# Kernel tuning notes

Hardware: AMD Instinct MI355X
Metric: run time of the kernel (lower is better)

## Reference

```python
import jax, jax.numpy as jnp
import numpy as np

B, N, E, H = 8, 1500, 3000, 256
HOPS = 3


def setup_inputs() -> dict:
    key = jax.random.key(0)
    ks = jax.random.split(key, 9)
    node_state = jax.random.normal(ks[0], (B, N, H), jnp.float32)
    edge_vec = jax.random.normal(ks[1], (B, E, H), jnp.float32)
    # sparse-ish 0/1 incidence matrices (avg ~3 nonzeros per row)
    node2edge = (jax.random.uniform(ks[2], (B, E, N)) < 0.002).astype(jnp.float32)
    edge2node = (jax.random.uniform(ks[3], (B, N, E)) < 0.002).astype(jnp.float32)
    s = 1.0 / np.sqrt(H).astype(np.float32)
    W_max = jax.random.uniform(ks[4], (H, H), jnp.float32, -s, s)        # linear_max, no bias
    W_fz = jax.random.uniform(ks[5], (4 * H, H), jnp.float32, -s, s)     # gated fusion
    b_fz = jnp.zeros((H,), jnp.float32)
    W_z = jax.random.uniform(ks[6], (2 * H, H), jnp.float32, -s, s)      # GRU gates, no bias
    W_r = jax.random.uniform(ks[7], (2 * H, H), jnp.float32, -s, s)
    W_t = jax.random.uniform(ks[8], (2 * H, H), jnp.float32, -s, s)
    return dict(node_state=node_state, edge_vec=edge_vec, node2edge=node2edge,
                edge2node=edge2node, W_max=W_max, W_fz=W_fz, b_fz=b_fz,
                W_z=W_z, W_r=W_r, W_t=W_t)


def _msg_pass(node_state, edge_vec, n2e, e2n):
    # n2e: (B,E,N), e2n: (B,N,E)
    edge_emb = jnp.einsum('ben,bnh->beh', n2e, node_state) + edge_vec   # (B,E,H)
    norm = jnp.sum(e2n, axis=2, keepdims=True) + 1.0                     # self-loop degree norm
    return (jnp.einsum('bne,beh->bnh', e2n, edge_emb) + node_state) / norm


def _gated_fusion(h, x, W_fz, b_fz):
    z = jax.nn.sigmoid(jnp.concatenate([h, x, h * x, h - x], -1) @ W_fz + b_fz)
    return (1.0 - z) * h + z * x


def _gru_step(h, x, W_z, W_r, W_t):
    hx = jnp.concatenate([h, x], -1)
    z = jax.nn.sigmoid(hx @ W_z)
    r = jax.nn.sigmoid(hx @ W_r)
    t = jnp.tanh(jnp.concatenate([r * h, x], -1) @ W_t)
    return (1.0 - z) * h + z * t


def reference(node_state, edge_vec, node2edge, edge2node, W_max, W_fz, b_fz, W_z, W_r, W_t):
    n2e_T = jnp.swapaxes(node2edge, 1, 2)   # (B,N,E)
    e2n_T = jnp.swapaxes(edge2node, 1, 2)   # (B,E,N)
    for _ in range(HOPS):
        bw = _msg_pass(node_state, edge_vec, node2edge, edge2node)
        fw = _msg_pass(node_state, edge_vec, e2n_T, n2e_T)
        agg = _gated_fusion(fw, bw, W_fz, b_fz)
        node_state = _gru_step(node_state, agg, W_z, W_r, W_t)
    # graph max pool: linear then max over nodes
    graph_embedding = jnp.max(node_state @ W_max, axis=1)[None]  # (1,B,H)
    return jnp.swapaxes(node_state, 0, 1), graph_embedding       # (N,B,H), (1,B,H)
```

## Files before the change

kernel.cpp:

```cpp
#include <hip/hip_runtime.h>
#include <hip/hip_bf16.h>
#include <stdint.h>

#define Bb 8
#define Nn 1500
#define Ee 3000
#define Hh 256
#define NHOPS 3
#define CAP 32
#define Mrows (Bb*Nn)
#define BE (Bb*Ee)
#define BN (Bb*Nn)

typedef __bf16 bf16x8 __attribute__((ext_vector_type(8)));
typedef float f32x4 __attribute__((ext_vector_type(4)));

__device__ __forceinline__ float sigmoidf_(float x){ return 1.f/(1.f+__expf(-x)); }

__device__ __forceinline__ unsigned short f2b(float f){
  union { float f; unsigned int u; } x; x.f = f;
  unsigned int r = (x.u + 0x7fffu + ((x.u >> 16) & 1u)) >> 16;
  return (unsigned short)r;
}
__device__ __forceinline__ float b2f(unsigned short u){
  union { unsigned int u; float f; } x; x.u = ((unsigned int)u) << 16;
  return x.f;
}
__device__ __forceinline__ ushort4 pack4(float4 v){
  return make_ushort4(f2b(v.x), f2b(v.y), f2b(v.z), f2b(v.w));
}
__device__ __forceinline__ float4 unpack4(ushort4 u){
  return make_float4(b2f(u.x), b2f(u.y), b2f(u.z), b2f(u.w));
}

#define GLL16(g, l) __builtin_amdgcn_global_load_lds( \
    (const __attribute__((address_space(1))) unsigned int*)(g), \
    (__attribute__((address_space(3))) unsigned int*)(l), 16, 0, 0)

__device__ __forceinline__ void elemscan(const float4* __restrict__ m4, int total4,
                                         int rowlen4, int R, int C,
                                         int* __restrict__ rowIdx, int* __restrict__ rowCnt,
                                         int* __restrict__ colIdx, int* __restrict__ colCnt,
                                         int t) {
  if (t >= total4) return;
  float4 v = m4[t];
  if (v.x == 0.f && v.y == 0.f && v.z == 0.f && v.w == 0.f) return;
  int g = t / rowlen4;
  int q = t - g * rowlen4;
  int b = g / R;
  int r = g - b * R;
  int cbase = q * 4;
  #pragma unroll
  for (int j = 0; j < 4; ++j) {
    float vv = (j == 0) ? v.x : (j == 1) ? v.y : (j == 2) ? v.z : v.w;
    if (vv != 0.f) {
      int c = cbase + j;
      int rs = atomicAdd(&rowCnt[g], 1);
      if (rs < CAP) rowIdx[(size_t)g * CAP + rs] = c;
      int cs = atomicAdd(&colCnt[b * C + c], 1);
      if (cs < CAP) colIdx[(size_t)(b * C + c) * CAP + cs] = r;
    }
  }
}

__global__ void preprocess_kernel(const float* __restrict__ n2e, const float* __restrict__ e2n,
                                  int* __restrict__ Aidx, int* __restrict__ cntA,
                                  int* __restrict__ Didx, int* __restrict__ cntD,
                                  int* __restrict__ Bidx, int* __restrict__ cntB,
                                  int* __restrict__ Cidx, int* __restrict__ cntC,
                                  const float* __restrict__ Wfz, const float* __restrict__ Wz,
                                  const float* __restrict__ Wr, const float* __restrict__ Wt,
                                  const float* __restrict__ Wmax,
                                  unsigned short* __restrict__ WfzT, unsigned short* __restrict__ WzrT,
                                  unsigned short* __restrict__ WtT, unsigned short* __restrict__ WmaxT,
                                  const float* __restrict__ in_ns, unsigned short* __restrict__ nsb,
                                  const float* __restrict__ in_ev, unsigned short* __restrict__ evb) {
  int bx = blockIdx.x;
  if (bx < 8790) {
    int t0 = bx * 1024 + threadIdx.x;
    #pragma unroll
    for (int rr = 0; rr < 4; ++rr)
      elemscan((const float4*)n2e, 9000000, 375, Ee, Nn,
               Aidx, cntA, Didx, cntD, t0 + rr * 256);
  } else if (bx < 17580) {
    int t0 = (bx - 8790) * 1024 + threadIdx.x;
    #pragma unroll
    for (int rr = 0; rr < 4; ++rr)
      elemscan((const float4*)e2n, 9000000, 750, Nn, Ee,
               Bidx, cntB, Cidx, cntC, t0 + rr * 256);
  } else if (bx < 20140) {
    int t = (bx - 17580) * 256 + threadIdx.x;
    if (t < 196608) {
      int n = t / 768, k = t % 768;
      float v;
      if (k < 256)      v = Wfz[k * 256 + n] + Wfz[(k + 768) * 256 + n];
      else if (k < 512) v = Wfz[k * 256 + n] - Wfz[(k + 512) * 256 + n];
      else              v = Wfz[k * 256 + n];
      WfzT[t] = f2b(v);
    } else if (t < 458752) {
      int u = t - 196608;
      int j = u >> 9, k = u & 511;
      float v = (j < 256) ? Wz[k * 256 + j] : Wr[k * 256 + (j - 256)];
      WzrT[u] = f2b(v);
    } else if (t < 589824) {
      int u = t - 458752;
      int n = u >> 9, k = u & 511;
      WtT[u] = f2b(Wt[k * 256 + n]);
    } else if (t < 655360) {
      int u = t - 589824;
      int n = u >> 8, k = u & 255;
      WmaxT[u] = f2b(Wmax[k * 256 + n]);
    }
  } else if (bx < 20890) {
    int t0 = (bx - 20140) * 1024 + threadIdx.x;
    #pragma unroll
    for (int r = 0; r < 4; ++r) {
      int t = t0 + r * 256;
      ((ushort4*)nsb)[t] = pack4(((const float4*)in_ns)[t]);
    }
  } else {
    int t0 = (bx - 20890) * 1024 + threadIdx.x;
    #pragma unroll
    for (int r = 0; r < 4; ++r) {
      int t = t0 + r * 256;
      ((ushort4*)evb)[t] = pack4(((const float4*)in_ev)[t]);
    }
  }
}

__device__ __forceinline__ void sort_one(int* pp, int c) {
  if (c > CAP) c = CAP;
  int v[CAP];
  for (int j = 0; j < c; ++j) v[j] = pp[j];
  for (int j = 1; j < c; ++j) { int key = v[j]; int k = j - 1;
    while (k >= 0 && v[k] > key) { v[k+1] = v[k]; --k; } v[k+1] = key; }
  for (int j = 0; j < c; ++j) pp[j] = v[j];
}
__global__ void sort4_kernel(int* __restrict__ Cidx, const int* __restrict__ cntC,
                             int* __restrict__ Didx, const int* __restrict__ cntD,
                             int* __restrict__ Aidx, const int* __restrict__ cntA,
                             int* __restrict__ Bidx, const int* __restrict__ cntB) {
  int i = blockIdx.x * 256 + threadIdx.x;
  if (i < BE) sort_one(Cidx + (size_t)i * CAP, cntC[i]);
  else if (i < BE + BN) { int k = i - BE; sort_one(Didx + (size_t)k * CAP, cntD[k]); }
  else if (i < 2 * BE + BN) { int k = i - BE - BN; sort_one(Aidx + (size_t)k * CAP, cntA[k]); }
  else if (i < 2 * BE + 2 * BN) { int k = i - 2 * BE - BN; sort_one(Bidx + (size_t)k * CAP, cntB[k]); }
}

__global__ void edge_kernel(const ushort4* __restrict__ evb4, const ushort4* __restrict__ nsb4,
                            const int* __restrict__ Aidx, const int* __restrict__ Acnt,
                            const int* __restrict__ Cidx, const int* __restrict__ Ccnt,
                            ushort4* __restrict__ eb4, ushort4* __restrict__ ef4) {
  int w = __builtin_amdgcn_readfirstlane((int)(threadIdx.x >> 6));
  int be = blockIdx.x * 4 + w;
  int lane = threadIdx.x & 63;
  int b = be / Ee;
  int cA = min(Acnt[be], CAP), cC = min(Ccnt[be], CAP);
  const int* pA = Aidx + (size_t)be * CAP;
  const int* pC = Cidx + (size_t)be * CAP;
  float4 ev = unpack4(evb4[(size_t)be * 64 + lane]);
  float4 sA = ev, sC = ev;
  for (int i = 0; i < cA; ++i) {
    int n = pA[i];
    float4 t = unpack4(nsb4[((size_t)b * Nn + n) * 64 + lane]);
    sA.x += t.x; sA.y += t.y; sA.z += t.z; sA.w += t.w;
  }
  for (int i = 0; i < cC; ++i) {
    int n = pC[i];
    float4 t = unpack4(nsb4[((size_t)b * Nn + n) * 64 + lane]);
    sC.x += t.x; sC.y += t.y; sC.z += t.z; sC.w += t.w;
  }
  eb4[(size_t)be * 64 + lane] = pack4(sA);
  ef4[(size_t)be * 64 + lane] = pack4(sC);
}

__global__ void node_kernel(const float4* __restrict__ nsin4,
                            const ushort4* __restrict__ eb4, const ushort4* __restrict__ ef4,
                            const int* __restrict__ Bidx, const int* __restrict__ Bcnt,
                            const int* __restrict__ Didx, const int* __restrict__ Dcnt,
                            ushort4* __restrict__ Xfz4, ushort4* __restrict__ Xzr4) {
  int w = __builtin_amdgcn_readfirstlane((int)(threadIdx.x >> 6));
  int bn = blockIdx.x * 4 + w;
  int lane = threadIdx.x & 63;
  int b = bn / Nn;
  int rB = Bcnt[bn], rD = Dcnt[bn];
  int cB = min(rB, CAP), cD = min(rD, CAP);
  const int* pB = Bidx + (size_t)bn * CAP;
  const int* pD = Didx + (size_t)bn * CAP;
  float4 h0 = nsin4[(size_t)bn * 64 + lane];
  float4 sb = h0, sf = h0;
  for (int i = 0; i < cB; ++i) {
    int e = pB[i];
    float4 t = unpack4(eb4[((size_t)b * Ee + e) * 64 + lane]);
    sb.x += t.x; sb.y += t.y; sb.z += t.z; sb.w += t.w;
  }
  for (int i = 0; i < cD; ++i) {
    int e = pD[i];
    float4 t = unpack4(ef4[((size_t)b * Ee + e) * 64 + lane]);
    sf.x += t.x; sf.y += t.y; sf.z += t.z; sf.w += t.w;
  }
  float ib = 1.f / (1.f + (float)rB), idf = 1.f / (1.f + (float)rD);
  sb.x *= ib; sb.y *= ib; sb.z *= ib; sb.w *= ib;
  sf.x *= idf; sf.y *= idf; sf.z *= idf; sf.w *= idf;
  float4 prod = make_float4(sf.x*sb.x, sf.y*sb.y, sf.z*sb.z, sf.w*sb.w);
  size_t m = bn;
  Xfz4[m * 192 +   0 + lane] = pack4(sf);
  Xfz4[m * 192 +  64 + lane] = pack4(sb);
  Xfz4[m * 192 + 128 + lane] = pack4(prod);
  Xzr4[m * 128 + lane] = pack4(h0);
}

#define EPI_NONE 0
#define EPI_FZ   1
#define EPI_ZR   2
#define EPI_GRU  3

template<int EPI, int LAST>
__global__ __launch_bounds__(512) void gemm_kernel(
    const unsigned short* __restrict__ A, const unsigned short* __restrict__ WT,
    int M, int K,
    float* __restrict__ outf, const float* __restrict__ bfz,
    unsigned short* __restrict__ Xzr, unsigned short* __restrict__ zbuf,
    unsigned short* __restrict__ Xt,
    const float* __restrict__ nsin, float* __restrict__ nsout,
    unsigned short* __restrict__ nsbout)
{
  __shared__ unsigned short As[128 * 64];
  __shared__ unsigned short Bs[64 * 64];
  int m0 = blockIdx.x * 128, n0 = blockIdx.y * 64;
  int tid = threadIdx.x;
  int lane = tid & 63;
  int wid = __builtin_amdgcn_readfirstlane(tid >> 6);
  int wm = wid >> 1, wn = wid & 1;
  int p = lane >> 4;
  int q = lane & 7;
  int lr = lane >> 3;
  f32x4 acc[2][2] = {};
  for (int k0 = 0; k0 < K; k0 += 64) {
    {
      int rl0 = wid * 16 + lr;
      int gm0 = m0 + rl0; if (gm0 > M - 1) gm0 = M - 1;
      GLL16(A + (size_t)gm0 * K + k0 + ((q ^ (rl0 & 7)) << 3), &As[(wid * 16) * 64]);
      int rl1 = rl0 + 8;
      int gm1 = m0 + rl1; if (gm1 > M - 1) gm1 = M - 1;
      GLL16(A + (size_t)gm1 * K + k0 + ((q ^ (rl1 & 7)) << 3), &As[(wid * 16 + 8) * 64]);
      int rb = wid * 8 + lr;
      GLL16(WT + (size_t)(n0 + rb) * K + k0 + ((q ^ (rb & 7)) << 3), &Bs[(wid * 8) * 64]);
    }
    __syncthreads();
    #pragma unroll
    for (int kk = 0; kk < 64; kk += 32) {
      int cq = (kk >> 3) + p;
      int ra0 = wm * 32 + (lane & 15);
      int ra1 = ra0 + 16;
      int rb0 = wn * 32 + (lane & 15);
      int rb1 = rb0 + 16;
      bf16x8 a0 = *(const bf16x8*)&As[ra0 * 64 + ((cq ^ (ra0 & 7)) << 3)];
      bf16x8 a1 = *(const bf16x8*)&As[ra1 * 64 + ((cq ^ (ra1 & 7)) << 3)];
      bf16x8 b0 = *(const bf16x8*)&Bs[rb0 * 64 + ((cq ^ (rb0 & 7)) << 3)];
      bf16x8 b1 = *(const bf16x8*)&Bs[rb1 * 64 + ((cq ^ (rb1 & 7)) << 3)];
      acc[0][0] = __builtin_amdgcn_mfma_f32_16x16x32_bf16(a0, b0, acc[0][0], 0, 0, 0);
      acc[0][1] = __builtin_amdgcn_mfma_f32_16x16x32_bf16(a0, b1, acc[0][1], 0, 0, 0);
      acc[1][0] = __builtin_amdgcn_mfma_f32_16x16x32_bf16(a1, b0, acc[1][0], 0, 0, 0);
      acc[1][1] = __builtin_amdgcn_mfma_f32_16x16x32_bf16(a1, b1, acc[1][1], 0, 0, 0);
    }
    __syncthreads();
  }
  #pragma unroll
  for (int mi = 0; mi < 2; ++mi)
  #pragma unroll
  for (int ni = 0; ni < 2; ++ni)
  #pragma unroll
  for (int j = 0; j < 4; ++j) {
    int m = m0 + wm * 32 + mi * 16 + p * 4 + j;
    int c = n0 + wn * 32 + ni * 16 + (lane & 15);
    if (m >= M) continue;
    float v = acc[mi][ni][j];
    if (EPI == EPI_NONE) {
      outf[(size_t)m * 256 + c] = v;
    } else if (EPI == EPI_FZ) {
      float z = sigmoidf_(v + bfz[c]);
      float fw = b2f(A[(size_t)m * K + c]);
      float bw = b2f(A[(size_t)m * K + 256 + c]);
      Xzr[(size_t)m * 512 + 256 + c] = f2b((1.f - z) * fw + z * bw);
    } else if (EPI == EPI_ZR) {
      float s = sigmoidf_(v);
      if (c < 256) {
        zbuf[(size_t)m * 256 + c] = f2b(s);
        Xt[(size_t)m * 512 + 256 + c] = A[(size_t)m * 512 + 256 + c];
      } else {
        int cz = c - 256;
        Xt[(size_t)m * 512 + cz] = f2b(s * nsin[(size_t)m * 256 + cz]);
      }
    } else {
      float t = tanhf(v);
      float zz = b2f(zbuf[(size_t)m * 256 + c]);
      float h = nsin[(size_t)m * 256 + c];
      float nh = (1.f - zz) * h + zz * t;
      nsbout[(size_t)m * 256 + c] = f2b(nh);
      if (LAST) {
        int bb = m / Nn, n = m - bb * Nn;
        nsout[((size_t)n * Bb + bb) * 256 + c] = nh;
      } else {
        nsout[(size_t)m * 256 + c] = nh;
      }
    }
  }
}

__global__ void maxpart_kernel(const float* __restrict__ tmp, float* __restrict__ part) {
  int bc = blockIdx.x;
  int b = bc / 12, ch = bc % 12;
  int h = threadIdx.x;
  float m = -1e30f;
  int nbase = ch * 125;
  for (int i = 0; i < 125; ++i)
    m = fmaxf(m, tmp[((size_t)b * Nn + nbase + i) * Hh + h]);
  part[(size_t)bc * Hh + h] = m;
}
__global__ void maxfin_kernel(const float* __restrict__ part, float* __restrict__ out) {
  int t = blockIdx.x * 256 + threadIdx.x;
  if (t >= Bb * Hh) return;
  int b = t / Hh, h = t % Hh;
  float m = -1e30f;
  for (int c = 0; c < 12; ++c) m = fmaxf(m, part[((size_t)b * 12 + c) * Hh + h]);
  out[(size_t)Nn * Bb * Hh + t] = m;
}

extern "C" void kernel_launch(void* const* d_in, const int* in_sizes, int n_in,
                              void* d_out, int out_size, void* d_ws, size_t ws_size,
                              hipStream_t stream) {
  const float* in_ns   = (const float*)d_in[0];
  const float* in_ev   = (const float*)d_in[1];
  const float* in_n2e  = (const float*)d_in[2];
  const float* in_e2n  = (const float*)d_in[3];
  const float* in_wmax = (const float*)d_in[4];
  const float* in_wfz  = (const float*)d_in[5];
  const float* in_bfz  = (const float*)d_in[6];
  const float* in_wz   = (const float*)d_in[7];
  const float* in_wr   = (const float*)d_in[8];
  const float* in_wt   = (const float*)d_in[9];
  float* out = (float*)d_out;

  char* base = (char*)d_ws;
  size_t off = 0;
  auto alloc = [&](size_t bytes) -> void* {
    void* r = base + off;
    off = (off + bytes + 255) & ~(size_t)255;
    return r;
  };
  int* cnts = (int*)alloc((size_t)(2 * BE + 2 * BN) * 4);
  int* cntC = cnts;
  int* cntD = cnts + BE;
  int* cntA = cnts + BE + BN;
  int* cntB = cnts + BE + BN + BE;
  int* Aidx = (int*)alloc((size_t)BE * CAP * 4);
  int* Bidx = (int*)alloc((size_t)BN * CAP * 4);
  int* Cidx = (int*)alloc((size_t)BE * CAP * 4);
  int* Didx = (int*)alloc((size_t)BN * CAP * 4);
  float* ns   = (float*)alloc((size_t)Mrows * Hh * 4);
  unsigned short* nsb = (unsigned short*)alloc((size_t)Mrows * Hh * 2);
  unsigned short* evb = (unsigned short*)alloc((size_t)BE * Hh * 2);
  unsigned short* eb = (unsigned short*)alloc((size_t)BE * Hh * 2);
  unsigned short* ef = (unsigned short*)alloc((size_t)BE * Hh * 2);
  float* gout = (float*)alloc((size_t)Mrows * 256 * 4);
  unsigned short* Xfz = (unsigned short*)alloc((size_t)Mrows * 768 * 2);
  unsigned short* Xzr = (unsigned short*)alloc((size_t)Mrows * 512 * 2);
  unsigned short* Xt  = (unsigned short*)alloc((size_t)Mrows * 512 * 2);
  unsigned short* zbuf = (unsigned short*)alloc((size_t)Mrows * 256 * 2);
  float* part = (float*)alloc((size_t)Bb * 12 * Hh * 4);
  unsigned short* WfzT  = (unsigned short*)alloc(256 * 768 * 2);
  unsigned short* WzrT  = (unsigned short*)alloc(512 * 512 * 2);
  unsigned short* WtT   = (unsigned short*)alloc(256 * 512 * 2);
  unsigned short* WmaxT = (unsigned short*)alloc(256 * 256 * 2);
  (void)ws_size; (void)in_sizes; (void)n_in; (void)out_size;

  hipMemsetAsync(cnts, 0, (size_t)(2 * BE + 2 * BN) * 4, stream);

  preprocess_kernel<<<22390, 256, 0, stream>>>(
      in_n2e, in_e2n,
      Aidx, cntA, Didx, cntD, Bidx, cntB, Cidx, cntC,
      in_wfz, in_wz, in_wr, in_wt, in_wmax,
      WfzT, WzrT, WtT, WmaxT,
      in_ns, nsb, in_ev, evb);
  sort4_kernel<<<(2 * BE + 2 * BN + 255) / 256, 256, 0, stream>>>(
      Cidx, cntC, Didx, cntD, Aidx, cntA, Bidx, cntB);

  dim3 gFZ(94, 4), gZR(94, 8), gT(94, 4);
  for (int hop = 0; hop < NHOPS; ++hop) {
    const float* nsin = (hop == 0) ? in_ns : ns;
    edge_kernel<<<BE / 4, 256, 0, stream>>>((const ushort4*)evb, (const ushort4*)nsb,
        Aidx, cntA, Cidx, cntC, (ushort4*)eb, (ushort4*)ef);
    node_kernel<<<BN / 4, 256, 0, stream>>>((const float4*)nsin,
        (const ushort4*)eb, (const ushort4*)ef,
        Bidx, cntB, Didx, cntD, (ushort4*)Xfz, (ushort4*)Xzr);
    gemm_kernel<EPI_FZ, 0><<<gFZ, 512, 0, stream>>>(Xfz, WfzT, Mrows, 768,
        nullptr, in_bfz, Xzr, nullptr, nullptr, nullptr, nullptr, nullptr);
    gemm_kernel<EPI_ZR, 0><<<gZR, 512, 0, stream>>>(Xzr, WzrT, Mrows, 512,
        nullptr, nullptr, nullptr, zbuf, Xt, nsin, nullptr, nullptr);
    if (hop < NHOPS - 1) {
      gemm_kernel<EPI_GRU, 0><<<gT, 512, 0, stream>>>(Xt, WtT, Mrows, 512,
          nullptr, nullptr, nullptr, zbuf, nullptr, nsin, ns, nsb);
    } else {
      gemm_kernel<EPI_GRU, 1><<<gT, 512, 0, stream>>>(Xt, WtT, Mrows, 512,
          nullptr, nullptr, nullptr, zbuf, nullptr, nsin, out, nsb);
    }
  }

  gemm_kernel<EPI_NONE, 0><<<gT, 512, 0, stream>>>(nsb, WmaxT, Mrows, 256,
      gout, nullptr, nullptr, nullptr, nullptr, nullptr, nullptr, nullptr);
  maxpart_kernel<<<Bb * 12, 256, 0, stream>>>(gout, part);
  maxfin_kernel<<<(Bb * Hh + 255) / 256, 256, 0, stream>>>(part, out);
}
```

Measured before the change: 436.3 us.

## Fuse max-pool into Wmax GEMM via atomics, split scan kernel, move agg copy

The final linear+max pool now reduces directly in the GEMM epilogue using order-preserving float keys and atomicMax, removing the full fp32 intermediate and the partial-max kernel. The incidence scan is split into a dedicated kernel that issues all four loads before processing, separate from weight/state conversion. The agg copy into Xt moves from the ZR epilogue to the FZ epilogue, avoiding a re-read of Xzr. These cut memory traffic and launches at the cost of atomic contention on a small key buffer.

```diff
diff --git a/kernel.cpp b/kernel.cpp
--- a/kernel.cpp
+++ b/kernel.cpp
@@ -11,6 +11,7 @@
 #define Mrows (Bb*Nn)
 #define BE (Bb*Ee)
 #define BN (Bb*Nn)
+#define TOTQ 9000000
 
 typedef __bf16 bf16x8 __attribute__((ext_vector_type(8)));
 typedef float f32x4 __attribute__((ext_vector_type(4)));
@@ -32,28 +33,38 @@
 __device__ __forceinline__ float4 unpack4(ushort4 u){
   return make_float4(b2f(u.x), b2f(u.y), b2f(u.z), b2f(u.w));
 }
+__device__ __forceinline__ unsigned fkey(float f){
+  unsigned u = __float_as_uint(f);
+  return (u & 0x80000000u) ? ~u : (u | 0x80000000u);
+}
 
 #define GLL16(g, l) __builtin_amdgcn_global_load_lds( \
     (const __attribute__((address_space(1))) unsigned int*)(g), \
     (__attribute__((address_space(3))) unsigned int*)(l), 16, 0, 0)
 
-__device__ __forceinline__ void elemscan(const float4* __restrict__ m4, int total4,
-                                         int rowlen4, int R, int C,
-                                         int* __restrict__ rowIdx, int* __restrict__ rowCnt,
-                                         int* __restrict__ colIdx, int* __restrict__ colCnt,
-                                         int t) {
-  if (t >= total4) return;
-  float4 v = m4[t];
-  if (v.x == 0.f && v.y == 0.f && v.z == 0.f && v.w == 0.f) return;
-  int g = t / rowlen4;
-  int q = t - g * rowlen4;
+__device__ __forceinline__ void scan_proc(float4 vv, int t,
+    int* __restrict__ Aidx, int* __restrict__ cntA, int* __restrict__ Didx, int* __restrict__ cntD,
+    int* __restrict__ Bidx, int* __restrict__ cntB, int* __restrict__ Cidx, int* __restrict__ cntC) {
+  if (vv.x == 0.f && vv.y == 0.f && vv.z == 0.f && vv.w == 0.f) return;
+  int *rowIdx, *rowCnt, *colIdx, *colCnt;
+  int g, q, R, C;
+  if (t < TOTQ) {
+    rowIdx = Aidx; rowCnt = cntA; colIdx = Didx; colCnt = cntD;
+    R = Ee; C = Nn;
+    g = t / 375; q = t - g * 375;
+  } else {
+    int tt = t - TOTQ;
+    rowIdx = Bidx; rowCnt = cntB; colIdx = Cidx; colCnt = cntC;
+    R = Nn; C = Ee;
+    g = tt / 750; q = tt - g * 750;
+  }
   int b = g / R;
   int r = g - b * R;
   int cbase = q * 4;
   #pragma unroll
   for (int j = 0; j < 4; ++j) {
-    float vv = (j == 0) ? v.x : (j == 1) ? v.y : (j == 2) ? v.z : v.w;
-    if (vv != 0.f) {
+    float vj = (j == 0) ? vv.x : (j == 1) ? vv.y : (j == 2) ? vv.z : vv.w;
+    if (vj != 0.f) {
       int c = cbase + j;
       int rs = atomicAdd(&rowCnt[g], 1);
       if (rs < CAP) rowIdx[(size_t)g * CAP + rs] = c;
@@ -63,33 +74,37 @@
   }
 }
 
-__global__ void preprocess_kernel(const float* __restrict__ n2e, const float* __restrict__ e2n,
-                                  int* __restrict__ Aidx, int* __restrict__ cntA,
-                                  int* __restrict__ Didx, int* __restrict__ cntD,
-                                  int* __restrict__ Bidx, int* __restrict__ cntB,
-                                  int* __restrict__ Cidx, int* __restrict__ cntC,
-                                  const float* __restrict__ Wfz, const float* __restrict__ Wz,
-                                  const float* __restrict__ Wr, const float* __restrict__ Wt,
-                                  const float* __restrict__ Wmax,
-                                  unsigned short* __restrict__ WfzT, unsigned short* __restrict__ WzrT,
-                                  unsigned short* __restrict__ WtT, unsigned short* __restrict__ WmaxT,
-                                  const float* __restrict__ in_ns, unsigned short* __restrict__ nsb,
-                                  const float* __restrict__ in_ev, unsigned short* __restrict__ evb) {
+__global__ void scan_kernel(const float4* __restrict__ n2e4, const float4* __restrict__ e2n4,
+                            int* __restrict__ Aidx, int* __restrict__ cntA,
+                            int* __restrict__ Didx, int* __restrict__ cntD,
+                            int* __restrict__ Bidx, int* __restrict__ cntB,
+                            int* __restrict__ Cidx, int* __restrict__ cntC) {
+  int t0 = blockIdx.x * 1024 + threadIdx.x;
+  float4 v[4];
+  int ts[4];
+  #pragma unroll
+  for (int r2 = 0; r2 < 4; ++r2) {
+    int t = t0 + r2 * 256;
+    ts[r2] = t;
+    const float4* p = (t < TOTQ) ? (n2e4 + t) : (e2n4 + (t - TOTQ));
+    v[r2] = (t < 2 * TOTQ) ? *p : make_float4(0.f, 0.f, 0.f, 0.f);
+  }
+  __builtin_amdgcn_sched_barrier(0);
+  #pragma unroll
+  for (int r2 = 0; r2 < 4; ++r2)
+    scan_proc(v[r2], ts[r2], Aidx, cntA, Didx, cntD, Bidx, cntB, Cidx, cntC);
+}
+
+__global__ void prep_kernel(const float* __restrict__ Wfz, const float* __restrict__ Wz,
+                            const float* __restrict__ Wr, const float* __restrict__ Wt,
+                            const float* __restrict__ Wmax,
+                            unsigned short* __restrict__ WfzT, unsigned short* __restrict__ WzrT,
+                            unsigned short* __restrict__ WtT, unsigned short* __restrict__ WmaxT,
+                            const float* __restrict__ in_ns, unsigned short* __restrict__ nsb,
+                            const float* __restrict__ in_ev, unsigned short* __restrict__ evb) {
   int bx = blockIdx.x;
-  if (bx < 8790) {
-    int t0 = bx * 1024 + threadIdx.x;
-    #pragma unroll
-    for (int rr = 0; rr < 4; ++rr)
-      elemscan((const float4*)n2e, 9000000, 375, Ee, Nn,
-               Aidx, cntA, Didx, cntD, t0 + rr * 256);
-  } else if (bx < 17580) {
-    int t0 = (bx - 8790) * 1024 + threadIdx.x;
-    #pragma unroll
-    for (int rr = 0; rr < 4; ++rr)
-      elemscan((const float4*)e2n, 9000000, 750, Nn, Ee,
-               Bidx, cntB, Cidx, cntC, t0 + rr * 256);
-  } else if (bx < 20140) {
-    int t = (bx - 17580) * 256 + threadIdx.x;
+  if (bx < 2560) {
+    int t = bx * 256 + threadIdx.x;
     if (t < 196608) {
       int n = t / 768, k = t % 768;
       float v;
@@ -111,15 +126,15 @@
       int n = u >> 8, k = u & 255;
       WmaxT[u] = f2b(Wmax[k * 256 + n]);
     }
-  } else if (bx < 20890) {
-    int t0 = (bx - 20140) * 1024 + threadIdx.x;
+  } else if (bx < 3310) {
+    int t0 = (bx - 2560) * 1024 + threadIdx.x;
     #pragma unroll
     for (int r = 0; r < 4; ++r) {
       int t = t0 + r * 256;
       ((ushort4*)nsb)[t] = pack4(((const float4*)in_ns)[t]);
     }
   } else {
-    int t0 = (bx - 20890) * 1024 + threadIdx.x;
+    int t0 = (bx - 3310) * 1024 + threadIdx.x;
     #pragma unroll
     for (int r = 0; r < 4; ++r) {
       int t = t0 + r * 256;
@@ -210,16 +225,16 @@
   Xzr4[m * 128 + lane] = pack4(h0);
 }
 
-#define EPI_NONE 0
 #define EPI_FZ   1
 #define EPI_ZR   2
 #define EPI_GRU  3
+#define EPI_MAX  4
 
 template<int EPI, int LAST>
 __global__ __launch_bounds__(512) void gemm_kernel(
     const unsigned short* __restrict__ A, const unsigned short* __restrict__ WT,
     int M, int K,
-    float* __restrict__ outf, const float* __restrict__ bfz,
+    unsigned* __restrict__ gkey, const float* __restrict__ bfz,
     unsigned short* __restrict__ Xzr, unsigned short* __restrict__ zbuf,
     unsigned short* __restrict__ Xt,
     const float* __restrict__ nsin, float* __restrict__ nsout,
@@ -266,6 +281,27 @@
     }
     __syncthreads();
   }
+  if (EPI == EPI_MAX) {
+    #pragma unroll
+    for (int mi = 0; mi < 2; ++mi)
+    #pragma unroll
+    for (int ni = 0; ni < 2; ++ni) {
+      int mb = m0 + wm * 32 + mi * 16 + p * 4;
+      int c = n0 + wn * 32 + ni * 16 + (lane & 15);
+      if (mb >= M) continue;
+      int b0 = mb / Nn, b3 = (mb + 3) / Nn;
+      if (b0 == b3) {
+        float mx = fmaxf(fmaxf(acc[mi][ni][0], acc[mi][ni][1]),
+                         fmaxf(acc[mi][ni][2], acc[mi][ni][3]));
+        atomicMax(&gkey[b0 * 256 + c], fkey(mx));
+      } else {
+        #pragma unroll
+        for (int j = 0; j < 4; ++j)
+          atomicMax(&gkey[((mb + j) / Nn) * 256 + c], fkey(acc[mi][ni][j]));
+      }
+    }
+    return;
+  }
   #pragma unroll
   for (int mi = 0; mi < 2; ++mi)
   #pragma unroll
@@ -276,18 +312,17 @@
     int c = n0 + wn * 32 + ni * 16 + (lane & 15);
     if (m >= M) continue;
     float v = acc[mi][ni][j];
-    if (EPI == EPI_NONE) {
-      outf[(size_t)m * 256 + c] = v;
-    } else if (EPI == EPI_FZ) {
+    if (EPI == EPI_FZ) {
       float z = sigmoidf_(v + bfz[c]);
       float fw = b2f(A[(size_t)m * K + c]);
       float bw = b2f(A[(size_t)m * K + 256 + c]);
-      Xzr[(size_t)m * 512 + 256 + c] = f2b((1.f - z) * fw + z * bw);
+      unsigned short agg = f2b((1.f - z) * fw + z * bw);
+      Xzr[(size_t)m * 512 + 256 + c] = agg;
+      Xt[(size_t)m * 512 + 256 + c] = agg;
     } else if (EPI == EPI_ZR) {
       float s = sigmoidf_(v);
       if (c < 256) {
         zbuf[(size_t)m * 256 + c] = f2b(s);
-        Xt[(size_t)m * 512 + 256 + c] = A[(size_t)m * 512 + 256 + c];
       } else {
         int cz = c - 256;
         Xt[(size_t)m * 512 + cz] = f2b(s * nsin[(size_t)m * 256 + cz]);
@@ -308,23 +343,12 @@
   }
 }
 
-__global__ void maxpart_kernel(const float* __restrict__ tmp, float* __restrict__ part) {
-  int bc = blockIdx.x;
-  int b = bc / 12, ch = bc % 12;
-  int h = threadIdx.x;
-  float m = -1e30f;
-  int nbase = ch * 125;
-  for (int i = 0; i < 125; ++i)
-    m = fmaxf(m, tmp[((size_t)b * Nn + nbase + i) * Hh + h]);
-  part[(size_t)bc * Hh + h] = m;
-}
-__global__ void maxfin_kernel(const float* __restrict__ part, float* __restrict__ out) {
+__global__ void maxfin_kernel(const unsigned* __restrict__ gkey, float* __restrict__ out) {
   int t = blockIdx.x * 256 + threadIdx.x;
   if (t >= Bb * Hh) return;
-  int b = t / Hh, h = t % Hh;
-  float m = -1e30f;
-  for (int c = 0; c < 12; ++c) m = fmaxf(m, part[((size_t)b * 12 + c) * Hh + h]);
-  out[(size_t)Nn * Bb * Hh + t] = m;
+  unsigned k = gkey[t];
+  unsigned u = (k & 0x80000000u) ? (k & 0x7fffffffu) : ~k;
+  out[(size_t)Nn * Bb * Hh + t] = __uint_as_float(u);
 }
 
 extern "C" void kernel_launch(void* const* d_in, const int* in_sizes, int n_in,
@@ -350,6 +374,7 @@
     return r;
   };
   int* cnts = (int*)alloc((size_t)(2 * BE + 2 * BN) * 4);
+  unsigned* gkey = (unsigned*)alloc(Bb * Hh * 4);
   int* cntC = cnts;
   int* cntD = cnts + BE;
   int* cntA = cnts + BE + BN;
@@ -363,23 +388,22 @@
   unsigned short* evb = (unsigned short*)alloc((size_t)BE * Hh * 2);
   unsigned short* eb = (unsigned short*)alloc((size_t)BE * Hh * 2);
   unsigned short* ef = (unsigned short*)alloc((size_t)BE * Hh * 2);
-  float* gout = (float*)alloc((size_t)Mrows * 256 * 4);
   unsigned short* Xfz = (unsigned short*)alloc((size_t)Mrows * 768 * 2);
   unsigned short* Xzr = (unsigned short*)alloc((size_t)Mrows * 512 * 2);
   unsigned short* Xt  = (unsigned short*)alloc((size_t)Mrows * 512 * 2);
   unsigned short* zbuf = (unsigned short*)alloc((size_t)Mrows * 256 * 2);
-  float* part = (float*)alloc((size_t)Bb * 12 * Hh * 4);
   unsigned short* WfzT  = (unsigned short*)alloc(256 * 768 * 2);
   unsigned short* WzrT  = (unsigned short*)alloc(512 * 512 * 2);
   unsigned short* WtT   = (unsigned short*)alloc(256 * 512 * 2);
   unsigned short* WmaxT = (unsigned short*)alloc(256 * 256 * 2);
   (void)ws_size; (void)in_sizes; (void)n_in; (void)out_size;
 
-  hipMemsetAsync(cnts, 0, (size_t)(2 * BE + 2 * BN) * 4, stream);
-
-  preprocess_kernel<<<22390, 256, 0, stream>>>(
-      in_n2e, in_e2n,
-      Aidx, cntA, Didx, cntD, Bidx, cntB, Cidx, cntC,
+  hipMemsetAsync(cnts, 0, (size_t)(2 * BE + 2 * BN) * 4 + (size_t)Bb * Hh * 4, stream);
+
+  scan_kernel<<<(2 * TOTQ + 1023) / 1024, 256, 0, stream>>>(
+      (const float4*)in_n2e, (const float4*)in_e2n,
+      Aidx, cntA, Didx, cntD, Bidx, cntB, Cidx, cntC);
+  prep_kernel<<<4810, 256, 0, stream>>>(
       in_wfz, in_wz, in_wr, in_wt, in_wmax,
       WfzT, WzrT, WtT, WmaxT,
       in_ns, nsb, in_ev, evb);
@@ -395,7 +419,7 @@
         (const ushort4*)eb, (const ushort4*)ef,
         Bidx, cntB, Didx, cntD, (ushort4*)Xfz, (ushort4*)Xzr);
     gemm_kernel<EPI_FZ, 0><<<gFZ, 512, 0, stream>>>(Xfz, WfzT, Mrows, 768,
-        nullptr, in_bfz, Xzr, nullptr, nullptr, nullptr, nullptr, nullptr);
+        nullptr, in_bfz, Xzr, nullptr, Xt, nullptr, nullptr, nullptr);
     gemm_kernel<EPI_ZR, 0><<<gZR, 512, 0, stream>>>(Xzr, WzrT, Mrows, 512,
         nullptr, nullptr, nullptr, zbuf, Xt, nsin, nullptr, nullptr);
     if (hop < NHOPS - 1) {
@@ -407,8 +431,7 @@
     }
   }
 
-  gemm_kernel<EPI_NONE, 0><<<gT, 512, 0, stream>>>(nsb, WmaxT, Mrows, 256,
-      gout, nullptr, nullptr, nullptr, nullptr, nullptr, nullptr, nullptr);
-  maxpart_kernel<<<Bb * 12, 256, 0, stream>>>(gout, part);
-  maxfin_kernel<<<(Bb * Hh + 255) / 256, 256, 0, stream>>>(part, out);
-}
+  gemm_kernel<EPI_MAX, 0><<<gT, 512, 0, stream>>>(nsb, WmaxT, Mrows, 256,
+      gkey, nullptr, nullptr, nullptr, nullptr, nullptr, nullptr, nullptr);
+  maxfin_kernel<<<(Bb * Hh + 255) / 256, 256, 0, stream>>>(gkey, out);
+}
```

Measured after the change: 443.1 us. Within noise of the previous version (+1.6%).
